# Kernel tuning notes

Measured on AMD Instinct MI355X. Metric: run time of the kernel, lower is better.

Reference implementation:

```python
import jax, jax.numpy as jnp
import numpy as np

EPS = float(np.finfo(np.float32).tiny)  # matches torch EPSILON
TAU = 0.1
K = 64  # self.k


def setup_inputs() -> dict:
    key = jax.random.key(0)
    k1, k2 = jax.random.split(key)
    bsz, Nmax, ensemble, train_ensemble = 64, 128, 2, 2
    scores = jax.random.normal(k1, (bsz, Nmax, Nmax, ensemble), dtype=jnp.float32)
    # Gumbel(0,1) noise, pre-sampled for determinism: g = -log(-log(U))
    u = jax.random.uniform(k2, (train_ensemble * bsz * ensemble, Nmax * Nmax),
                           dtype=jnp.float32, minval=1e-7, maxval=1.0 - 1e-7)
    gumbel = -jnp.log(-jnp.log(u))
    return {"scores": scores, "gumbel": gumbel, "train_ensemble": train_ensemble}


def reference(scores, gumbel, train_ensemble):
    # policy == 'global_topk_directed'
    bsz, Nmax, _, ensemble = scores.shape
    local_k = min(K, Nmax * Nmax)
    # (bsz, Nmax, Nmax, E) -> (bsz*E, Nmax^2)
    flat = scores.transpose(0, 3, 1, 2).reshape(bsz * ensemble, Nmax * Nmax)
    flat = jnp.tile(flat, (train_ensemble, 1)) + gumbel

    zeros = jnp.zeros_like(flat)

    def step(carry, _):
        f, khot, onehot = carry
        f = f + jnp.log(jnp.maximum(1.0 - onehot, EPS))
        onehot = jax.nn.softmax(f / TAU, axis=1)
        return (f, khot + onehot, onehot), None

    (flat, khot, _), _ = jax.lax.scan(step, (flat, zeros, zeros), None, length=local_k)

    # hard: straight-through k-hot via top-k scatter
    _, ind = jax.lax.top_k(khot, local_k)  # (R, local_k)
    rows = jnp.arange(khot.shape[0])[:, None]
    khot_hard = jnp.zeros_like(khot).at[rows, ind].set(1.0)
    res = khot_hard - jax.lax.stop_gradient(khot) + khot

    new_mask = res.reshape(train_ensemble, bsz, ensemble, Nmax, Nmax).transpose(0, 1, 3, 4, 2)
    return new_mask
```

## Files before the change

kernel.cpp:

```cpp
#include <hip/hip_runtime.h>
#include <math.h>


#define BLOCK   1024
#define NWAVES  16
#define M_ELEMS 16384
#define EPT     16
#define KSEL    64
#define NCAND   256
#define CPL     4
#define NBINS   4096
#define THRESH  (M_ELEMS - NCAND)
#define C10     14.42695019f

template <int CTRL, int RM = 0xF>
__device__ __forceinline__ float dpp_f(float x, float identity) {
    return __int_as_float(__builtin_amdgcn_update_dpp(
        __float_as_int(identity), __float_as_int(x), CTRL, RM, 0xF, false));
}
template <int CTRL, int RM = 0xF>
__device__ __forceinline__ unsigned dpp_u(unsigned x, unsigned identity) {
    return (unsigned)__builtin_amdgcn_update_dpp(
        (int)identity, (int)x, CTRL, RM, 0xF, false);
}
__device__ __forceinline__ float wave_sum_bcast(float x) {
    x += dpp_f<0x111>(x, 0.0f);
    x += dpp_f<0x112>(x, 0.0f);
    x += dpp_f<0x114>(x, 0.0f);
    x += dpp_f<0x118>(x, 0.0f);
    x += dpp_f<0x142>(x, 0.0f);
    x += dpp_f<0x143>(x, 0.0f);
    return __int_as_float(__builtin_amdgcn_readlane(__float_as_int(x), 63));
}
__device__ __forceinline__ float wave_fmax_bcast(float x) {
    x = fmaxf(x, dpp_f<0x111>(x, -INFINITY));
    x = fmaxf(x, dpp_f<0x112>(x, -INFINITY));
    x = fmaxf(x, dpp_f<0x114>(x, -INFINITY));
    x = fmaxf(x, dpp_f<0x118>(x, -INFINITY));
    x = fmaxf(x, dpp_f<0x142>(x, -INFINITY));
    x = fmaxf(x, dpp_f<0x143>(x, -INFINITY));
    return __int_as_float(__builtin_amdgcn_readlane(__float_as_int(x), 63));
}
__device__ __forceinline__ unsigned wave_prefix_incl(unsigned x) {
    x += dpp_u<0x111>(x, 0u);
    x += dpp_u<0x112>(x, 0u);
    x += dpp_u<0x114>(x, 0u);
    x += dpp_u<0x118>(x, 0u);
    x += dpp_u<0x142, 0xA>(x, 0u);
    x += dpp_u<0x143, 0xC>(x, 0u);
    return x;
}

__global__ __launch_bounds__(BLOCK, 4) void gumbel_topk_kernel(
    const float* __restrict__ scores,
    const float* __restrict__ gumbel,
    float* __restrict__ out)
{
    const int tid  = threadIdx.x;
    const int lane = tid & 63;
    const int wid  = tid >> 6;
    const int bid = blockIdx.x;
    const int r   = (gridDim.x == 256) ? (((bid & 127) << 1) | (bid >> 7)) : bid;
    const int t_ = r >> 7;
    const int be = r & 127;
    const int b  = be >> 1;
    const int e  = be & 1;

    __shared__ unsigned int          hist[NBINS];
    __shared__ __align__(16) float    exbuf[NCAND];
    __shared__ __align__(16) unsigned idxbuf[NCAND];
    __shared__ unsigned int          wofs[NWAVES];
    __shared__ unsigned int          cutbin;
    __shared__ unsigned int          candcnt;

    float* orow = out + (size_t)(t_ * 64 + b) * (M_ELEMS * 2) + e;

    float fv[EPT];
    {
        const float* gum = gumbel + (size_t)r * M_ELEMS;
        const float* scb = scores + (size_t)b * (M_ELEMS * 2);
        #pragma unroll
        for (int g = 0; g < 4; ++g) {
            const int mb = (tid << 2) + (g << 12);
            const float4 gv = *reinterpret_cast<const float4*>(&gum[mb]);
            const float4 sa = *reinterpret_cast<const float4*>(&scb[(size_t)mb * 2]);
            const float4 sb = *reinterpret_cast<const float4*>(&scb[(size_t)mb * 2 + 4]);
            float s0, s1, s2, s3;
            if (e == 0) { s0 = sa.x; s1 = sa.z; s2 = sb.x; s3 = sb.z; }
            else        { s0 = sa.y; s1 = sa.w; s2 = sb.y; s3 = sb.w; }
            fv[g * 4 + 0] = s0 + gv.x;
            fv[g * 4 + 1] = s1 + gv.y;
            fv[g * 4 + 2] = s2 + gv.z;
            fv[g * 4 + 3] = s3 + gv.w;
        }
    }
    #pragma unroll
    for (int k = 0; k < NBINS / BLOCK; ++k) hist[tid + k * BLOCK] = 0u;
    __syncthreads();

    #pragma unroll
    for (int k = 0; k < EPT; ++k) {
        const unsigned u  = __float_as_uint(fv[k]);
        const unsigned tk = u ^ (unsigned)(((int)u >> 31) | 0x80000000);
        atomicAdd(&hist[tk >> 20], 1u);
    }
    __syncthreads();

    if (wid == 0) {
        unsigned part = 0;
        #pragma unroll 8
        for (int j = 0; j < 64; ++j)
            part += hist[(lane << 6) + ((j + lane) & 63)];
        const unsigned P = wave_prefix_incl(part);
        const unsigned long long mk = __ballot(P >= THRESH);
        const int L = __builtin_ctzll(mk);
        const unsigned base = (L > 0)
            ? (unsigned)__builtin_amdgcn_readlane((int)P, L - 1) : 0u;
        const unsigned h2 = hist[(L << 6) + lane];
        const unsigned p2 = wave_prefix_incl(h2) + base;
        const unsigned long long mk2 = __ballot(p2 >= THRESH);
        const int j2 = __builtin_ctzll(mk2);
        if (lane == 0) {
            cutbin  = (unsigned)((L << 6) + j2 + 1);
            candcnt = M_ELEMS - (unsigned)__builtin_amdgcn_readlane((int)p2, j2);
        }
    }
    __syncthreads();
    const unsigned cutKey = cutbin << 20;
    const unsigned nc     = candcnt;

    unsigned mycnt = 0, hitm = 0;
    #pragma unroll
    for (int k = 0; k < EPT; ++k) {
        const unsigned u  = __float_as_uint(fv[k]);
        const unsigned tk = u ^ (unsigned)(((int)u >> 31) | 0x80000000);
        const bool c = tk >= cutKey;
        hitm |= (c ? 1u : 0u) << k;
        mycnt += c ? 1u : 0u;
    }
    const unsigned inc = wave_prefix_incl(mycnt);
    if (lane == 63) wofs[wid] = inc;
    __syncthreads();
    unsigned wbase = 0;
    #pragma unroll
    for (int i = 0; i < NWAVES; ++i) wbase += (i < wid) ? wofs[i] : 0u;
    unsigned slot = wbase + inc - mycnt;
    #pragma unroll
    for (int k = 0; k < EPT; ++k) {
        if ((hitm >> k) & 1u) {
            exbuf[slot]  = fv[k];
            idxbuf[slot] = (unsigned)((tid << 2) + (k & 3) + ((k >> 2) << 12));
            ++slot;
        }
    }
    if ((unsigned)tid >= nc && tid < NCAND) {
        exbuf[tid]  = -INFINITY;
        idxbuf[tid] = 0x7fffffffu;
    }
    __syncthreads();

    if (wid == 0) {
        float cf[CPL], cex[CPL], ckh[CPL];
        #pragma unroll
        for (int k = 0; k < CPL; ++k) cf[k] = exbuf[lane + (k << 6)];
        float cmax = fmaxf(fmaxf(cf[0], cf[1]), fmaxf(cf[2], cf[3]));
        cmax = wave_fmax_bcast(cmax);
        const float nbw = fmaf(-cmax, C10, 60.0f);
        #pragma unroll
        for (int k = 0; k < CPL; ++k) {
            cex[k] = __builtin_amdgcn_exp2f(fmaf(cf[k], C10, nbw));
            ckh[k] = 0.0f;
        }
        for (int it = 0; it < KSEL; ++it) {
            float gsum = wave_sum_bcast((cex[0] + cex[1]) + (cex[2] + cex[3]));
            const int eb = (int)((__float_as_uint(gsum) >> 23) & 0xFF);
            if (eb < 127 + 50) {
                int sh = 314 - eb;
                if (sh > 254) sh = 254;
                const float s = __uint_as_float((unsigned)sh << 23);
                #pragma unroll
                for (int k = 0; k < CPL; ++k) cex[k] *= s;
                gsum = wave_sum_bcast((cex[0] + cex[1]) + (cex[2] + cex[3]));
                if (!(gsum > 0.0f)) gsum = INFINITY;
            }
            const float rsum = __builtin_amdgcn_rcpf(gsum);
            #pragma unroll
            for (int k = 0; k < CPL; ++k) {
                ckh[k] = fmaf(cex[k], rsum, ckh[k]);
                const float t  = fmaf(-cex[k], rsum, 1.0f);
                const float t2 = t * t;
                const float t4 = t2 * t2;
                const float t8 = t4 * t4;
                cex[k] = cex[k] * t8 * t2;
            }
        }
        #pragma unroll
        for (int k = 0; k < CPL; ++k) exbuf[lane + (k << 6)] = ckh[k];
    } else {
        for (int m = tid - 64; m < M_ELEMS; m += BLOCK - 64)
            orow[(size_t)m * 2] = 0.0f;
    }
    __syncthreads();

    if (tid < NCAND) {
        const float    myv = exbuf[tid];
        const unsigned myi = idxbuf[tid];
        unsigned rank = 0;
        #pragma unroll 8
        for (int j = 0; j < NCAND; j += 4) {
            const float4 v  = *reinterpret_cast<const float4*>(&exbuf[j]);
            const uint4  ii = *reinterpret_cast<const uint4*>(&idxbuf[j]);
            rank += (v.x > myv || (v.x == myv && ii.x < myi)) ? 1u : 0u;
            rank += (v.y > myv || (v.y == myv && ii.y < myi)) ? 1u : 0u;
            rank += (v.z > myv || (v.z == myv && ii.z < myi)) ? 1u : 0u;
            rank += (v.w > myv || (v.w == myv && ii.w < myi)) ? 1u : 0u;
        }
        if (rank < KSEL && myi < M_ELEMS)
            orow[(size_t)myi * 2] = 1.0f;
    }
}

extern "C" void kernel_launch(void* const* d_in, const int* in_sizes, int n_in,
                              void* d_out, int out_size, void* d_ws, size_t ws_size,
                              hipStream_t stream) {
    const float* scores = (const float*)d_in[0];
    const float* gumbel = (const float*)d_in[1];
    float* out = (float*)d_out;
    const int rows = in_sizes[1] / M_ELEMS;
    gumbel_topk_kernel<<<rows, BLOCK, 0, stream>>>(scores, gumbel, out);
}
```

Measured before the change: 33.27 us.

## Split screening and softmax iteration into two kernels via workspace candidates

```diff
diff --git a/kernel.cpp b/kernel.cpp
--- a/kernel.cpp
+++ b/kernel.cpp
@@ -2,7 +2,6 @@
 #include <math.h>
 
 
-#define BLOCK   1024
 #define NWAVES  16
 #define M_ELEMS 16384
 #define EPT     16
@@ -51,27 +50,27 @@
     return x;
 }
 
-__global__ __launch_bounds__(BLOCK, 4) void gumbel_topk_kernel(
+__global__ __launch_bounds__(1024, 4) void screen_kernel(
     const float* __restrict__ scores,
     const float* __restrict__ gumbel,
+    float* __restrict__ cand_f,
+    unsigned* __restrict__ cand_i,
     float* __restrict__ out)
 {
     const int tid  = threadIdx.x;
     const int lane = tid & 63;
     const int wid  = tid >> 6;
     const int bid = blockIdx.x;
-    const int r   = (gridDim.x == 256) ? (((bid & 127) << 1) | (bid >> 7)) : bid;
+    const int r   = ((bid & 127) << 1) | (bid >> 7);
     const int t_ = r >> 7;
     const int be = r & 127;
     const int b  = be >> 1;
     const int e  = be & 1;
 
-    __shared__ unsigned int          hist[NBINS];
-    __shared__ __align__(16) float    exbuf[NCAND];
-    __shared__ __align__(16) unsigned idxbuf[NCAND];
-    __shared__ unsigned int          wofs[NWAVES];
-    __shared__ unsigned int          cutbin;
-    __shared__ unsigned int          candcnt;
+    __shared__ unsigned int hist[NBINS];
+    __shared__ unsigned int wofs[NWAVES];
+    __shared__ unsigned int cutbin;
+    __shared__ unsigned int candcnt;
 
     float* orow = out + (size_t)(t_ * 64 + b) * (M_ELEMS * 2) + e;
 
@@ -95,7 +94,7 @@
         }
     }
     #pragma unroll
-    for (int k = 0; k < NBINS / BLOCK; ++k) hist[tid + k * BLOCK] = 0u;
+    for (int k = 0; k < NBINS / 1024; ++k) hist[tid + k * 1024] = 0u;
     __syncthreads();
 
     #pragma unroll
@@ -145,27 +144,55 @@
     #pragma unroll
     for (int i = 0; i < NWAVES; ++i) wbase += (i < wid) ? wofs[i] : 0u;
     unsigned slot = wbase + inc - mycnt;
+    float*    cfr = cand_f + (size_t)r * NCAND;
+    unsigned* cir = cand_i + (size_t)r * NCAND;
     #pragma unroll
     for (int k = 0; k < EPT; ++k) {
         if ((hitm >> k) & 1u) {
-            exbuf[slot]  = fv[k];
-            idxbuf[slot] = (unsigned)((tid << 2) + (k & 3) + ((k >> 2) << 12));
+            cfr[slot] = fv[k];
+            cir[slot] = (unsigned)((tid << 2) + (k & 3) + ((k >> 2) << 12));
             ++slot;
         }
     }
     if ((unsigned)tid >= nc && tid < NCAND) {
-        exbuf[tid]  = -INFINITY;
-        idxbuf[tid] = 0x7fffffffu;
-    }
-    __syncthreads();
+        cfr[tid] = -INFINITY;
+        cir[tid] = 0x7fffffffu;
+    }
+
+    #pragma unroll
+    for (int k = 0; k < EPT; ++k)
+        orow[(size_t)(tid + (k << 10)) * 2] = 0.0f;
+}
+
+__global__ __launch_bounds__(256, 8) void dyn_kernel(
+    const float* __restrict__ cand_f,
+    const unsigned* __restrict__ cand_i,
+    float* __restrict__ out)
+{
+    const int tid  = threadIdx.x;
+    const int lane = tid & 63;
+    const int wid  = tid >> 6;
+    const int r    = blockIdx.x;
+    const int t_ = r >> 7;
+    const int be = r & 127;
+    const int b  = be >> 1;
+    const int e  = be & 1;
+
+    __shared__ __align__(16) float    khbuf[NCAND];
+    __shared__ __align__(16) unsigned idxb[NCAND];
+
+    float* orow = out + (size_t)(t_ * 64 + b) * (M_ELEMS * 2) + e;
+
+    idxb[tid] = cand_i[(size_t)r * NCAND + tid];
 
     if (wid == 0) {
         float cf[CPL], cex[CPL], ckh[CPL];
         #pragma unroll
-        for (int k = 0; k < CPL; ++k) cf[k] = exbuf[lane + (k << 6)];
+        for (int k = 0; k < CPL; ++k)
+            cf[k] = cand_f[(size_t)r * NCAND + lane + (k << 6)];
         float cmax = fmaxf(fmaxf(cf[0], cf[1]), fmaxf(cf[2], cf[3]));
         cmax = wave_fmax_bcast(cmax);
-        const float nbw = fmaf(-cmax, C10, 60.0f);
+        const float nbw = fmaf(-cmax, C10, 100.0f);
         #pragma unroll
         for (int k = 0; k < CPL; ++k) {
             cex[k] = __builtin_amdgcn_exp2f(fmaf(cf[k], C10, nbw));
@@ -174,8 +201,8 @@
         for (int it = 0; it < KSEL; ++it) {
             float gsum = wave_sum_bcast((cex[0] + cex[1]) + (cex[2] + cex[3]));
             const int eb = (int)((__float_as_uint(gsum) >> 23) & 0xFF);
-            if (eb < 127 + 50) {
-                int sh = 314 - eb;
+            if (eb < 127 + 10) {
+                int sh = 354 - eb;
                 if (sh > 254) sh = 254;
                 const float s = __uint_as_float((unsigned)sh << 23);
                 #pragma unroll
@@ -195,29 +222,24 @@
             }
         }
         #pragma unroll
-        for (int k = 0; k < CPL; ++k) exbuf[lane + (k << 6)] = ckh[k];
-    } else {
-        for (int m = tid - 64; m < M_ELEMS; m += BLOCK - 64)
-            orow[(size_t)m * 2] = 0.0f;
-    }
-    __syncthreads();
-
-    if (tid < NCAND) {
-        const float    myv = exbuf[tid];
-        const unsigned myi = idxbuf[tid];
-        unsigned rank = 0;
-        #pragma unroll 8
-        for (int j = 0; j < NCAND; j += 4) {
-            const float4 v  = *reinterpret_cast<const float4*>(&exbuf[j]);
-            const uint4  ii = *reinterpret_cast<const uint4*>(&idxbuf[j]);
-            rank += (v.x > myv || (v.x == myv && ii.x < myi)) ? 1u : 0u;
-            rank += (v.y > myv || (v.y == myv && ii.y < myi)) ? 1u : 0u;
-            rank += (v.z > myv || (v.z == myv && ii.z < myi)) ? 1u : 0u;
-            rank += (v.w > myv || (v.w == myv && ii.w < myi)) ? 1u : 0u;
-        }
-        if (rank < KSEL && myi < M_ELEMS)
-            orow[(size_t)myi * 2] = 1.0f;
-    }
+        for (int k = 0; k < CPL; ++k) khbuf[lane + (k << 6)] = ckh[k];
+    }
+    __syncthreads();
+
+    const float    myv = khbuf[tid];
+    const unsigned myi = idxb[tid];
+    unsigned rank = 0;
+    #pragma unroll 8
+    for (int j = 0; j < NCAND; j += 4) {
+        const float4 v  = *reinterpret_cast<const float4*>(&khbuf[j]);
+        const uint4  ii = *reinterpret_cast<const uint4*>(&idxb[j]);
+        rank += (v.x > myv || (v.x == myv && ii.x < myi)) ? 1u : 0u;
+        rank += (v.y > myv || (v.y == myv && ii.y < myi)) ? 1u : 0u;
+        rank += (v.z > myv || (v.z == myv && ii.z < myi)) ? 1u : 0u;
+        rank += (v.w > myv || (v.w == myv && ii.w < myi)) ? 1u : 0u;
+    }
+    if (rank < KSEL && myi < M_ELEMS)
+        orow[(size_t)myi * 2] = 1.0f;
 }
 
 extern "C" void kernel_launch(void* const* d_in, const int* in_sizes, int n_in,
@@ -227,5 +249,8 @@
     const float* gumbel = (const float*)d_in[1];
     float* out = (float*)d_out;
     const int rows = in_sizes[1] / M_ELEMS;
-    gumbel_topk_kernel<<<rows, BLOCK, 0, stream>>>(scores, gumbel, out);
-}
+    float*    cand_f = (float*)d_ws;
+    unsigned* cand_i = (unsigned*)d_ws + (size_t)rows * NCAND;
+    screen_kernel<<<rows, 1024, 0, stream>>>(scores, gumbel, cand_f, cand_i, out);
+    dyn_kernel<<<rows, 256, 0, stream>>>(cand_f, cand_i, out);
+}
```

After: 36.54 us. 1.1x slower.

## Process both ensemble rows per block with shared score loads and vector zeroing

Applied to the files above, without the earlier changes.

```diff
diff --git a/kernel.cpp b/kernel.cpp
--- a/kernel.cpp
+++ b/kernel.cpp
@@ -2,8 +2,6 @@
 #include <math.h>
 
 
-#define BLOCK   1024
-#define NWAVES  16
 #define M_ELEMS 16384
 #define EPT     16
 #define KSEL    64
@@ -51,7 +49,7 @@
     return x;
 }
 
-__global__ __launch_bounds__(BLOCK, 4) void gumbel_topk_kernel(
+__global__ __launch_bounds__(1024, 4) void gumbel_pair_kernel(
     const float* __restrict__ scores,
     const float* __restrict__ gumbel,
     float* __restrict__ out)
@@ -59,113 +57,129 @@
     const int tid  = threadIdx.x;
     const int lane = tid & 63;
     const int wid  = tid >> 6;
-    const int bid = blockIdx.x;
-    const int r   = (gridDim.x == 256) ? (((bid & 127) << 1) | (bid >> 7)) : bid;
-    const int t_ = r >> 7;
-    const int be = r & 127;
-    const int b  = be >> 1;
-    const int e  = be & 1;
-
-    __shared__ unsigned int          hist[NBINS];
-    __shared__ __align__(16) float    exbuf[NCAND];
-    __shared__ __align__(16) unsigned idxbuf[NCAND];
-    __shared__ unsigned int          wofs[NWAVES];
-    __shared__ unsigned int          cutbin;
-    __shared__ unsigned int          candcnt;
-
-    float* orow = out + (size_t)(t_ * 64 + b) * (M_ELEMS * 2) + e;
-
-    float fv[EPT];
+    const int pair = blockIdx.x;
+    const int t_ = pair >> 6;
+    const int b  = pair & 63;
+    const int r0 = t_ * 128 + 2 * b;
+
+    __shared__ unsigned int           hist[2][NBINS];
+    __shared__ __align__(16) float    cfb[2][NCAND];
+    __shared__ __align__(16) unsigned cib[2][NCAND];
+    __shared__ unsigned int           wofs[2][16];
+    __shared__ unsigned int           cutb[2], ccnt[2];
+
+    float* obase = out + (size_t)(t_ * 64 + b) * (M_ELEMS * 2);
+
+    const float4 z4 = make_float4(0.f, 0.f, 0.f, 0.f);
+    #pragma unroll
+    for (int g = 0; g < 8; ++g)
+        *reinterpret_cast<float4*>(&obase[(size_t)(tid + (g << 10)) << 2]) = z4;
+
+    float fv0[EPT], fv1[EPT];
     {
-        const float* gum = gumbel + (size_t)r * M_ELEMS;
+        const float* g0  = gumbel + (size_t)r0 * M_ELEMS;
+        const float* g1  = g0 + M_ELEMS;
         const float* scb = scores + (size_t)b * (M_ELEMS * 2);
         #pragma unroll
         for (int g = 0; g < 4; ++g) {
             const int mb = (tid << 2) + (g << 12);
-            const float4 gv = *reinterpret_cast<const float4*>(&gum[mb]);
+            const float4 ga = *reinterpret_cast<const float4*>(&g0[mb]);
+            const float4 gb = *reinterpret_cast<const float4*>(&g1[mb]);
             const float4 sa = *reinterpret_cast<const float4*>(&scb[(size_t)mb * 2]);
             const float4 sb = *reinterpret_cast<const float4*>(&scb[(size_t)mb * 2 + 4]);
-            float s0, s1, s2, s3;
-            if (e == 0) { s0 = sa.x; s1 = sa.z; s2 = sb.x; s3 = sb.z; }
-            else        { s0 = sa.y; s1 = sa.w; s2 = sb.y; s3 = sb.w; }
-            fv[g * 4 + 0] = s0 + gv.x;
-            fv[g * 4 + 1] = s1 + gv.y;
-            fv[g * 4 + 2] = s2 + gv.z;
-            fv[g * 4 + 3] = s3 + gv.w;
-        }
-    }
-    #pragma unroll
-    for (int k = 0; k < NBINS / BLOCK; ++k) hist[tid + k * BLOCK] = 0u;
+            fv0[g * 4 + 0] = sa.x + ga.x;   fv1[g * 4 + 0] = sa.y + gb.x;
+            fv0[g * 4 + 1] = sa.z + ga.y;   fv1[g * 4 + 1] = sa.w + gb.y;
+            fv0[g * 4 + 2] = sb.x + ga.z;   fv1[g * 4 + 2] = sb.y + gb.z;
+            fv0[g * 4 + 3] = sb.z + ga.w;   fv1[g * 4 + 3] = sb.w + gb.w;
+        }
+    }
+    {
+        unsigned* hf = &hist[0][0];
+        #pragma unroll
+        for (int k = 0; k < (2 * NBINS) / 1024; ++k) hf[tid + (k << 10)] = 0u;
+    }
     __syncthreads();
 
     #pragma unroll
     for (int k = 0; k < EPT; ++k) {
-        const unsigned u  = __float_as_uint(fv[k]);
-        const unsigned tk = u ^ (unsigned)(((int)u >> 31) | 0x80000000);
-        atomicAdd(&hist[tk >> 20], 1u);
-    }
-    __syncthreads();
-
-    if (wid == 0) {
+        const unsigned u0 = __float_as_uint(fv0[k]);
+        const unsigned k0 = u0 ^ (unsigned)(((int)u0 >> 31) | 0x80000000);
+        atomicAdd(&hist[0][k0 >> 20], 1u);
+        const unsigned u1 = __float_as_uint(fv1[k]);
+        const unsigned k1 = u1 ^ (unsigned)(((int)u1 >> 31) | 0x80000000);
+        atomicAdd(&hist[1][k1 >> 20], 1u);
+    }
+    __syncthreads();
+
+    if (wid < 2) {
+        const unsigned* h = hist[wid];
         unsigned part = 0;
         #pragma unroll 8
         for (int j = 0; j < 64; ++j)
-            part += hist[(lane << 6) + ((j + lane) & 63)];
+            part += h[(lane << 6) + ((j + lane) & 63)];
         const unsigned P = wave_prefix_incl(part);
         const unsigned long long mk = __ballot(P >= THRESH);
         const int L = __builtin_ctzll(mk);
         const unsigned base = (L > 0)
             ? (unsigned)__builtin_amdgcn_readlane((int)P, L - 1) : 0u;
-        const unsigned h2 = hist[(L << 6) + lane];
+        const unsigned h2 = h[(L << 6) + lane];
         const unsigned p2 = wave_prefix_incl(h2) + base;
         const unsigned long long mk2 = __ballot(p2 >= THRESH);
         const int j2 = __builtin_ctzll(mk2);
         if (lane == 0) {
-            cutbin  = (unsigned)((L << 6) + j2 + 1);
-            candcnt = M_ELEMS - (unsigned)__builtin_amdgcn_readlane((int)p2, j2);
-        }
-    }
-    __syncthreads();
-    const unsigned cutKey = cutbin << 20;
-    const unsigned nc     = candcnt;
-
-    unsigned mycnt = 0, hitm = 0;
+            cutb[wid] = (unsigned)((L << 6) + j2 + 1);
+            ccnt[wid] = M_ELEMS - (unsigned)__builtin_amdgcn_readlane((int)p2, j2);
+        }
+    }
+    __syncthreads();
+    const unsigned cut0 = cutb[0] << 20, nc0 = ccnt[0];
+    const unsigned cut1 = cutb[1] << 20, nc1 = ccnt[1];
+
+    unsigned c0 = 0, h0 = 0, c1 = 0, h1 = 0;
     #pragma unroll
     for (int k = 0; k < EPT; ++k) {
-        const unsigned u  = __float_as_uint(fv[k]);
-        const unsigned tk = u ^ (unsigned)(((int)u >> 31) | 0x80000000);
-        const bool c = tk >= cutKey;
-        hitm |= (c ? 1u : 0u) << k;
-        mycnt += c ? 1u : 0u;
-    }
-    const unsigned inc = wave_prefix_incl(mycnt);
-    if (lane == 63) wofs[wid] = inc;
-    __syncthreads();
-    unsigned wbase = 0;
-    #pragma unroll
-    for (int i = 0; i < NWAVES; ++i) wbase += (i < wid) ? wofs[i] : 0u;
-    unsigned slot = wbase + inc - mycnt;
+        const unsigned u0 = __float_as_uint(fv0[k]);
+        const unsigned k0 = u0 ^ (unsigned)(((int)u0 >> 31) | 0x80000000);
+        const bool s0 = k0 >= cut0;
+        h0 |= (s0 ? 1u : 0u) << k;  c0 += s0 ? 1u : 0u;
+        const unsigned u1 = __float_as_uint(fv1[k]);
+        const unsigned k1 = u1 ^ (unsigned)(((int)u1 >> 31) | 0x80000000);
+        const bool s1 = k1 >= cut1;
+        h1 |= (s1 ? 1u : 0u) << k;  c1 += s1 ? 1u : 0u;
+    }
+    const unsigned inc0 = wave_prefix_incl(c0);
+    const unsigned inc1 = wave_prefix_incl(c1);
+    if (lane == 63) { wofs[0][wid] = inc0; wofs[1][wid] = inc1; }
+    __syncthreads();
+    unsigned wb0 = 0, wb1 = 0;
+    #pragma unroll
+    for (int i = 0; i < 16; ++i) {
+        wb0 += (i < wid) ? wofs[0][i] : 0u;
+        wb1 += (i < wid) ? wofs[1][i] : 0u;
+    }
+    unsigned s0 = wb0 + inc0 - c0;
+    unsigned s1 = wb1 + inc1 - c1;
     #pragma unroll
     for (int k = 0; k < EPT; ++k) {
-        if ((hitm >> k) & 1u) {
-            exbuf[slot]  = fv[k];
-            idxbuf[slot] = (unsigned)((tid << 2) + (k & 3) + ((k >> 2) << 12));
-            ++slot;
-        }
-    }
-    if ((unsigned)tid >= nc && tid < NCAND) {
-        exbuf[tid]  = -INFINITY;
-        idxbuf[tid] = 0x7fffffffu;
-    }
-    __syncthreads();
-
-    if (wid == 0) {
+        const unsigned mi = (unsigned)((tid << 2) + (k & 3) + ((k >> 2) << 12));
+        if ((h0 >> k) & 1u) { cfb[0][s0] = fv0[k]; cib[0][s0] = mi; ++s0; }
+        if ((h1 >> k) & 1u) { cfb[1][s1] = fv1[k]; cib[1][s1] = mi; ++s1; }
+    }
+    if ((unsigned)tid >= nc0 && tid < NCAND) {
+        cfb[0][tid] = -INFINITY;  cib[0][tid] = 0x7fffffffu;
+    }
+    if ((unsigned)tid >= nc1 && tid < NCAND) {
+        cfb[1][tid] = -INFINITY;  cib[1][tid] = 0x7fffffffu;
+    }
+    __syncthreads();
+
+    if (wid < 2) {
         float cf[CPL], cex[CPL], ckh[CPL];
         #pragma unroll
-        for (int k = 0; k < CPL; ++k) cf[k] = exbuf[lane + (k << 6)];
+        for (int k = 0; k < CPL; ++k) cf[k] = cfb[wid][lane + (k << 6)];
         float cmax = fmaxf(fmaxf(cf[0], cf[1]), fmaxf(cf[2], cf[3]));
         cmax = wave_fmax_bcast(cmax);
-        const float nbw = fmaf(-cmax, C10, 60.0f);
+        const float nbw = fmaf(-cmax, C10, 100.0f);
         #pragma unroll
         for (int k = 0; k < CPL; ++k) {
             cex[k] = __builtin_amdgcn_exp2f(fmaf(cf[k], C10, nbw));
@@ -174,8 +188,8 @@
         for (int it = 0; it < KSEL; ++it) {
             float gsum = wave_sum_bcast((cex[0] + cex[1]) + (cex[2] + cex[3]));
             const int eb = (int)((__float_as_uint(gsum) >> 23) & 0xFF);
-            if (eb < 127 + 50) {
-                int sh = 314 - eb;
+            if (eb < 127 + 10) {
+                int sh = 354 - eb;
                 if (sh > 254) sh = 254;
                 const float s = __uint_as_float((unsigned)sh << 23);
                 #pragma unroll
@@ -195,28 +209,27 @@
             }
         }
         #pragma unroll
-        for (int k = 0; k < CPL; ++k) exbuf[lane + (k << 6)] = ckh[k];
-    } else {
-        for (int m = tid - 64; m < M_ELEMS; m += BLOCK - 64)
-            orow[(size_t)m * 2] = 0.0f;
-    }
-    __syncthreads();
-
-    if (tid < NCAND) {
-        const float    myv = exbuf[tid];
-        const unsigned myi = idxbuf[tid];
+        for (int k = 0; k < CPL; ++k) cfb[wid][lane + (k << 6)] = ckh[k];
+    }
+    __syncthreads();
+
+    if (tid < 2 * NCAND) {
+        const int      sel = tid >> 8;
+        const int      j0  = tid & 255;
+        const float    myv = cfb[sel][j0];
+        const unsigned myi = cib[sel][j0];
         unsigned rank = 0;
         #pragma unroll 8
         for (int j = 0; j < NCAND; j += 4) {
-            const float4 v  = *reinterpret_cast<const float4*>(&exbuf[j]);
-            const uint4  ii = *reinterpret_cast<const uint4*>(&idxbuf[j]);
+            const float4 v  = *reinterpret_cast<const float4*>(&cfb[sel][j]);
+            const uint4  ii = *reinterpret_cast<const uint4*>(&cib[sel][j]);
             rank += (v.x > myv || (v.x == myv && ii.x < myi)) ? 1u : 0u;
             rank += (v.y > myv || (v.y == myv && ii.y < myi)) ? 1u : 0u;
             rank += (v.z > myv || (v.z == myv && ii.z < myi)) ? 1u : 0u;
             rank += (v.w > myv || (v.w == myv && ii.w < myi)) ? 1u : 0u;
         }
         if (rank < KSEL && myi < M_ELEMS)
-            orow[(size_t)myi * 2] = 1.0f;
+            obase[((size_t)myi << 1) + sel] = 1.0f;
     }
 }
 
@@ -226,6 +239,7 @@
     const float* scores = (const float*)d_in[0];
     const float* gumbel = (const float*)d_in[1];
     float* out = (float*)d_out;
-    const int rows = in_sizes[1] / M_ELEMS;
-    gumbel_topk_kernel<<<rows, BLOCK, 0, stream>>>(scores, gumbel, out);
-}
+    const int rows  = in_sizes[1] / M_ELEMS;
+    const int pairs = rows / 2;
+    gumbel_pair_kernel<<<pairs, 1024, 0, stream>>>(scores, gumbel, out);
+}
```

New measurement: 37.17 us. 1.12x slower.
